# Kernel tuning notes

Hardware: AMD Instinct MI355X
Metric: run time of the kernel (lower is better)

Reference implementation:

```python
import jax, jax.numpy as jnp
import numpy as np

OBS, H, F1, A, T, B = 128, 128, 256, 18, 128, 1024


def _ln(x, w, b, eps=1e-5):
    mu = jnp.mean(x, -1, keepdims=True)
    xc = x - mu
    var = jnp.mean(xc * xc, -1, keepdims=True)
    return xc * jax.lax.rsqrt(var + eps) * w + b


def _features(x, w1, b1, w2, b2, lnw, lnb):
    h = jax.nn.relu(x @ w1.T + b1)      # [N, 256]
    h = h @ w2.T + b2                   # [N, 128]
    return jax.nn.relu(_ln(h, lnw, lnb))


def _masked_lstm(xs, ds, h0, c0, wih, whh, b):
    # xs: [T,B,H], ds: [T,B] float; PyTorch gate order i,f,g,o
    def step(carry, inp):
        h, c = carry
        xt, dt = inp
        m = (1.0 - dt)[:, None]
        h = h * m
        c = c * m
        g = xt @ wih.T + h @ whh.T + b  # [B, 4H]
        i, f, gg, o = jnp.split(g, 4, axis=-1)
        c = jax.nn.sigmoid(f) * c + jax.nn.sigmoid(i) * jnp.tanh(gg)
        h = jax.nn.sigmoid(o) * jnp.tanh(c)
        return (h, c), h
    (hT, cT), hs = jax.lax.scan(step, (h0, c0), (xs, ds))
    return hs, hT, cT


def setup_inputs() -> dict:
    key = jax.random.key(0)
    ks = iter(jax.random.split(key, 64))
    p = lambda shape, s=0.05: jax.random.normal(next(ks), shape, jnp.float32) * s
    inp = {
        'x': jax.random.normal(next(ks), (T * B, OBS), jnp.float32),
        'actor_h': jnp.zeros((1, B, H), jnp.float32),
        'actor_c': jnp.zeros((1, B, H), jnp.float32),
        'critic_h': jnp.zeros((1, B, H), jnp.float32),
        'critic_c': jnp.zeros((1, B, H), jnp.float32),
        'done': jax.random.randint(next(ks), (T * B,), 0, 2, jnp.int32),
        'action': jax.random.randint(next(ks), (T * B,), 0, A, jnp.int64),
        # actor params
        'af_w1': p((F1, OBS)), 'af_b1': p((F1,)),
        'af_w2': p((H, F1)), 'af_b2': p((H,)),
        'af_lnw': jnp.ones((H,), jnp.float32), 'af_lnb': jnp.zeros((H,), jnp.float32),
        'a_wih': p((4 * H, H)), 'a_whh': p((4 * H, H)), 'a_b': p((4 * H,)),
        'a_lnw': jnp.ones((H,), jnp.float32), 'a_lnb': jnp.zeros((H,), jnp.float32),
        'a_hw': p((A, H)), 'a_hb': p((A,)),
        # critic params
        'cf_w1': p((F1, OBS)), 'cf_b1': p((F1,)),
        'cf_w2': p((H, F1)), 'cf_b2': p((H,)),
        'cf_lnw': jnp.ones((H,), jnp.float32), 'cf_lnb': jnp.zeros((H,), jnp.float32),
        'c_wih': p((4 * H, H)), 'c_whh': p((4 * H, H)), 'c_b': p((4 * H,)),
        'c_lnw': jnp.ones((H,), jnp.float32), 'c_lnb': jnp.zeros((H,), jnp.float32),
        'c_hw': p((1, H)), 'c_hb': p((1,)),
    }
    return inp


def reference(x, actor_h, actor_c, critic_h, critic_c,
              af_w1, af_b1, af_w2, af_b2, af_lnw, af_lnb,
              a_wih, a_whh, a_b, a_lnw, a_lnb, a_hw, a_hb,
              cf_w1, cf_b1, cf_w2, cf_b2, cf_lnw, cf_lnb,
              c_wih, c_whh, c_b, c_lnw, c_lnb, c_hw, c_hb,
              done, action):
    bsz = actor_h.shape[1]
    ds = done.astype(jnp.float32).reshape(-1, bsz)  # [T, B]

    # actor branch
    af = _features(x, af_w1, af_b1, af_w2, af_b2, af_lnw, af_lnb).reshape(-1, bsz, H)
    hs, ahT, acT = _masked_lstm(af, ds, actor_h[0], actor_c[0], a_wih, a_whh, a_b)
    ah = _ln(hs.reshape(-1, H), a_lnw, a_lnb)
    logits = ah @ a_hw.T + a_hb                     # [N, A]
    logp_all = jax.nn.log_softmax(logits)
    logp = jnp.take_along_axis(logp_all, action[:, None], axis=1)[:, 0]
    entropy = -jnp.sum(jnp.exp(logp_all) * logp_all, axis=-1)

    # critic branch
    cf = _features(x, cf_w1, cf_b1, cf_w2, cf_b2, cf_lnw, cf_lnb).reshape(-1, bsz, H)
    cs, chT, ccT = _masked_lstm(cf, ds, critic_h[0], critic_c[0], c_wih, c_whh, c_b)
    ch = _ln(cs.reshape(-1, H), c_lnw, c_lnb)
    value = ch @ c_hw.T + c_hb                      # [N, 1]

    return (action, logp, entropy, value,
            ahT[None], acT[None], chT[None], ccT[None])
```

## Files before the change

### kernel.cpp

```cpp
#include <hip/hip_runtime.h>
#include <stdint.h>
#include <stddef.h>

#define OBS 128
#define F1D 256
#define HD  128
#define NA  18
#define TT  128
#define BB  1024
#define NN  (TT*BB)
#define LOG2E 1.442695041f

typedef __attribute__((ext_vector_type(8))) short short8;
typedef __attribute__((ext_vector_type(4))) float f32x4;

__device__ __forceinline__ unsigned short f2bf(float f) {
  union { float f; uint32_t u; } v; v.f = f;
  uint32_t u = v.u;
  u += 0x7fffu + ((u >> 16) & 1u);
  return (unsigned short)(u >> 16);
}
__device__ __forceinline__ float bf2f(uint32_t hu) {
  union { uint32_t u; float f; } v; v.u = hu << 16;
  return v.f;
}
__device__ __forceinline__ uint32_t pk2(float lo, float hi) {
  uint32_t r;
  asm("v_cvt_pk_bf16_f32 %0, %1, %2" : "=v"(r) : "v"(lo), "v"(hi));
  return r;
}
__device__ __forceinline__ f32x4 mfma16(short8 a, short8 b, f32x4 c) {
  return __builtin_amdgcn_mfma_f32_16x16x32_bf16(a, b, c, 0, 0, 0);
}
__device__ __forceinline__ short8 cvt8(const float* p, float sc) {
  float4 a = *(const float4*)p;
  float4 b = *(const float4*)(p + 4);
  union { uint32_t u[4]; short8 s; } o;
  o.u[0] = pk2(a.x*sc, a.y*sc);
  o.u[1] = pk2(a.z*sc, a.w*sc);
  o.u[2] = pk2(b.x*sc, b.y*sc);
  o.u[3] = pk2(b.z*sc, b.w*sc);
  return o.s;
}
__device__ __forceinline__ short8 pin(short8 v) {
  int4 i = *(int4*)&v;
  asm volatile("" : "+v"(i.x), "+v"(i.y), "+v"(i.z), "+v"(i.w));
  return *(short8*)&i;
}

__global__ __launch_bounds__(512, 2) void feat_kernel(
    const float* __restrict__ x,
    const float* __restrict__ aw1, const float* __restrict__ ab1,
    const float* __restrict__ aw2, const float* __restrict__ ab2,
    const float* __restrict__ aflnw, const float* __restrict__ aflnb,
    const float* __restrict__ cw1, const float* __restrict__ cb1,
    const float* __restrict__ cw2, const float* __restrict__ cb2,
    const float* __restrict__ cflnw, const float* __restrict__ cflnb,
    unsigned short* __restrict__ featg)
{
  int g = blockIdx.x;
  int br = g >> 7;
  int chunk = g & 127;
  int base8 = chunk * 8;

  const float* w1  = br ? cw1 : aw1;
  const float* b1  = br ? cb1 : ab1;
  const float* w2  = br ? cw2 : aw2;
  const float* b2  = br ? cb2 : ab2;
  const float* flw = br ? cflnw : aflnw;
  const float* flb = br ? cflnb : aflnb;
  unsigned short* feat = featg + (size_t)br * NN * HD;

  __shared__ __align__(16) char smemA[51200];

  int tid = threadIdx.x;
  int w = tid >> 6, lane = tid & 63, q = lane >> 4, ln = lane & 15;
  int team = tid >> 8, t_tid = tid & 255, w4 = w & 3;

  unsigned short* xst  = (unsigned short*)smemA + team*4096;
  unsigned short* h1st = (unsigned short*)(smemA + 16384) + team*8192;
  float*          lnst = (float*)(smemA + 49152) + team*256;

  short8 b1f[4][4]; float b1v[4];
  #pragma unroll
  for (int ct = 0; ct < 4; ++ct) {
    int nn = w4*64 + ct*16 + ln;
    b1v[ct] = b1[nn];
    #pragma unroll
    for (int kf = 0; kf < 4; ++kf)
      b1f[ct][kf] = pin(cvt8(&w1[nn*OBS + kf*32 + q*8], 1.0f));
  }
  short8 b2f[2][8]; float b2v[2], lwv[2], lbv[2];
  #pragma unroll
  for (int nt = 0; nt < 2; ++nt) {
    int nn = w4*32 + nt*16 + ln;
    b2v[nt] = b2[nn]; lwv[nt] = flw[nn]; lbv[nt] = flb[nn];
    #pragma unroll
    for (int kf = 0; kf < 8; ++kf)
      b2f[nt][kf] = pin(cvt8(&w2[nn*F1D + kf*32 + q*8], 1.0f));
  }
  float4 xr[4];
  #pragma unroll
  for (int s = 0; s < 4; ++s) {
    int e4 = t_tid + s*256;
    int r = e4 >> 5, c4 = e4 & 31;
    size_t grow = (size_t)(team*4 + (r>>3))*BB + base8 + (r&7);
    xr[s] = ((const float4*)x)[grow*32 + c4];
  }
  for (int j = 0; j < 16; ++j) {
    int jj = j*2 + team;
    #pragma unroll
    for (int s = 0; s < 4; ++s) {
      int e = (t_tid + s*256) * 4;
      int r = e >> 7, k = e & 127;
      int ad = r*128 + ((((k>>3) ^ (r&15)) << 3)) + (k&7);
      uint2 d;
      d.x = pk2(xr[s].x, xr[s].y);
      d.y = pk2(xr[s].z, xr[s].w);
      *(uint2*)&xst[ad] = d;
    }
    __syncthreads();
    {
      int jjn = (j < 15) ? jj + 2 : jj;
      #pragma unroll
      for (int s = 0; s < 4; ++s) {
        int e4 = t_tid + s*256;
        int r = e4 >> 5, c4 = e4 & 31;
        size_t grow = (size_t)(jjn*4 + (r>>3))*BB + base8 + (r&7);
        xr[s] = ((const float4*)x)[grow*32 + c4];
      }
    }
    short8 af[2][4];
    #pragma unroll
    for (int mt = 0; mt < 2; ++mt)
      #pragma unroll
      for (int kf = 0; kf < 4; ++kf)
        af[mt][kf] = *(const short8*)&xst[(mt*16 + ln)*128 + ((((kf<<2)|q) ^ ln) << 3)];
    #pragma unroll
    for (int ct = 0; ct < 4; ++ct) {
      int nn = w4*64 + ct*16 + ln;
      #pragma unroll
      for (int mt = 0; mt < 2; ++mt) {
        f32x4 acc = {b1v[ct], b1v[ct], b1v[ct], b1v[ct]};
        #pragma unroll
        for (int kf = 0; kf < 4; ++kf) acc = mfma16(af[mt][kf], b1f[ct][kf], acc);
        float v0 = acc[0] > 0.0f ? acc[0] : 0.0f;
        float v1 = acc[1] > 0.0f ? acc[1] : 0.0f;
        float v2 = acc[2] > 0.0f ? acc[2] : 0.0f;
        float v3 = acc[3] > 0.0f ? acc[3] : 0.0f;
        uint32_t p01 = pk2(v0, v1), p23 = pk2(v2, v3);
        int r0 = mt*16 + q*4;
        h1st[(r0+0)*256 + (((nn>>3) ^ ((r0+0)&15)) << 3) + (nn&7)] = (unsigned short)p01;
        h1st[(r0+1)*256 + (((nn>>3) ^ ((r0+1)&15)) << 3) + (nn&7)] = (unsigned short)(p01 >> 16);
        h1st[(r0+2)*256 + (((nn>>3) ^ ((r0+2)&15)) << 3) + (nn&7)] = (unsigned short)p23;
        h1st[(r0+3)*256 + (((nn>>3) ^ ((r0+3)&15)) << 3) + (nn&7)] = (unsigned short)(p23 >> 16);
      }
    }
    __syncthreads();
    f32x4 acc2[2][2];
    #pragma unroll
    for (int mt = 0; mt < 2; ++mt) {
      short8 ah[8];
      #pragma unroll
      for (int kf = 0; kf < 8; ++kf)
        ah[kf] = *(const short8*)&h1st[(mt*16 + ln)*256 + ((((kf<<2)|q) ^ ln) << 3)];
      #pragma unroll
      for (int nt = 0; nt < 2; ++nt) {
        f32x4 acc = {b2v[nt], b2v[nt], b2v[nt], b2v[nt]};
        #pragma unroll
        for (int kf = 0; kf < 8; ++kf) acc = mfma16(ah[kf], b2f[nt][kf], acc);
        acc2[nt][mt] = acc;
      }
    }
    #pragma unroll
    for (int mt = 0; mt < 2; ++mt)
      #pragma unroll
      for (int rg = 0; rg < 4; ++rg) {
        float s = acc2[0][mt][rg] + acc2[1][mt][rg];
        float ssq = acc2[0][mt][rg]*acc2[0][mt][rg] + acc2[1][mt][rg]*acc2[1][mt][rg];
        #pragma unroll
        for (int m = 1; m < 16; m <<= 1) { s += __shfl_xor(s, m); ssq += __shfl_xor(ssq, m); }
        if (ln == 0) {
          int r = mt*16 + q*4 + rg;
          lnst[r*8 + w4*2]     = s;
          lnst[r*8 + w4*2 + 1] = ssq;
        }
      }
    __syncthreads();
    #pragma unroll
    for (int mt = 0; mt < 2; ++mt)
      #pragma unroll
      for (int rg = 0; rg < 4; ++rg) {
        int r = mt*16 + q*4 + rg;
        float4 p0 = *(const float4*)&lnst[r*8];
        float4 p1 = *(const float4*)&lnst[r*8 + 4];
        float S  = p0.x + p0.z + p1.x + p1.z;
        float SS = p0.y + p0.w + p1.y + p1.w;
        float mu = S * (1.0f/128.0f);
        float var = SS * (1.0f/128.0f) - mu*mu;
        float rstd = rsqrtf(var + 1e-5f);
        size_t grow = (size_t)(jj*4 + (r>>3))*BB + base8 + (r&7);
        float t0 = (acc2[0][mt][rg] - mu) * rstd * lwv[0] + lbv[0];
        float t1 = (acc2[1][mt][rg] - mu) * rstd * lwv[1] + lbv[1];
        if (t0 < 0.0f) t0 = 0.0f;
        if (t1 < 0.0f) t1 = 0.0f;
        uint32_t p = pk2(t0, t1);
        unsigned short* fp = &feat[grow*HD + w4*32 + ln];
        fp[0]  = (unsigned short)p;
        fp[16] = (unsigned short)(p >> 16);
      }
    __syncthreads();
  }
}

__global__ __launch_bounds__(512, 2) void lstm_head_kernel(
    const int* __restrict__ done, const int* __restrict__ action,
    const float* __restrict__ awih, const float* __restrict__ awhh,
    const float* __restrict__ a_b,
    const float* __restrict__ alnw, const float* __restrict__ alnb,
    const float* __restrict__ ahw, const float* __restrict__ ahb,
    const float* __restrict__ cwih, const float* __restrict__ cwhh,
    const float* __restrict__ c_b,
    const float* __restrict__ clnw, const float* __restrict__ clnb,
    const float* __restrict__ chw, const float* __restrict__ chb,
    const float* __restrict__ ah0, const float* __restrict__ ac0,
    const float* __restrict__ ch0, const float* __restrict__ cc0,
    unsigned short* __restrict__ featg, float* __restrict__ dout)
{
  int g = blockIdx.x;
  int br = g >> 7;
  int chunk = g & 127;
  int base8 = chunk * 8;

  const float* wih = br ? cwih : awih;
  const float* whh = br ? cwhh : awhh;
  const float* gb  = br ? c_b : a_b;
  const float* h0  = br ? ch0 : ah0;
  const float* c0  = br ? cc0 : ac0;
  unsigned short* feat = featg + (size_t)br * NN * HD;

  __shared__ __align__(16) char smemC[51200];
  __shared__ float mls[(TT+1)*8];
  __shared__ unsigned short hlds[2][8*128];
  __shared__ float pa[HD], pb[HD], cws[HD];
  __shared__ float hbl[NA];
  __shared__ float cbsS;
  __shared__ int flagS;

  int tid = threadIdx.x;
  int w = tid >> 6, lane = tid & 63, q = lane >> 4, ln = lane & 15;

  int n = w*16 + ln;
  {
    short8 bfr[4][8]; float bias[4];
    #pragma unroll
    for (int g4 = 0; g4 < 4; ++g4) {
      int gn = g4*128 + n;
      float sc = (g4 == 2) ? -2.0f*LOG2E : -LOG2E;
      bias[g4] = gb[gn] * sc;
      #pragma unroll
      for (int kf = 0; kf < 8; ++kf) {
        const float* src = (kf < 4) ? &wih[gn*HD + kf*32 + q*8]
                                    : &whh[gn*HD + (kf-4)*32 + q*8];
        bfr[g4][kf] = pin(cvt8(src, sc));
      }
    }
    for (int i = tid; i < (TT+1)*8; i += 512)
      mls[i] = (i < TT*8) ? 1.0f - (float)done[(i>>3)*BB + base8 + (i&7)] : 1.0f;

    const int loff = (base8 + (ln>>1))*HD + q*8;
    int soff[2], hoffw[2], haddr[4];
    #pragma unroll
    for (int j = 0; j < 2; ++j) {
      int r = q*2 + j;
      soff[j]  = (base8 + r)*HD + n;
      hoffw[j] = r*128 + (((n>>3) ^ r) << 3) + (n&7);
    }
    #pragma unroll
    for (int kf = 0; kf < 4; ++kf) {
      int rr = ln >> 1;
      haddr[kf] = rr*128 + ((((kf<<2)|q) ^ rr) << 3);
    }
    float hp[2], cp[2]; unsigned short hu_prev[2];
    #pragma unroll
    for (int j = 0; j < 2; ++j) {
      int b = base8 + q*2 + j;
      hp[j] = h0[b*HD + n];
      cp[j] = c0[b*HD + n];
      hu_prev[j] = 0;
    }
    __syncthreads();
    short8 afr[4], nfr[4];
    #pragma unroll
    for (int kf = 0; kf < 4; ++kf)
      afr[kf] = *(const short8*)&feat[loff + kf*32];
    {
      float m0 = mls[q*2], m1 = mls[q*2 + 1];
      cp[0] *= m0; cp[1] *= m1;
      uint32_t hpk = pk2(hp[0]*m0, hp[1]*m1);
      hlds[0][hoffw[0]] = (unsigned short)hpk;
      hlds[0][hoffw[1]] = (unsigned short)(hpk >> 16);
    }
    __syncthreads();

#define LSTM_STEP(TTT, CUR, NXT, HB)                                           \
  {                                                                            \
    short8 hfr[4];                                                             \
    _Pragma("unroll")                                                          \
    for (int kf = 0; kf < 4; ++kf)                                             \
      hfr[kf] = *(const short8*)&hlds[HB][haddr[kf]];                          \
    {                                                                          \
      int tp = (TTT) > 0 ? (TTT) - 1 : 0;                                      \
      unsigned short* sq = feat + (size_t)tp * (BB*HD);                        \
      sq[soff[0]] = hu_prev[0];                                                \
      sq[soff[1]] = hu_prev[1];                                                \
    }                                                                          \
    int tn = ((TTT) + 1 < TT) ? (TTT) + 1 : TT - 1;                            \
    const unsigned short* fq = feat + (size_t)tn * (BB*HD);                    \
    _Pragma("unroll")                                                          \
    for (int kf = 0; kf < 4; ++kf)                                             \
      NXT[kf] = *(const short8*)&fq[loff + kf*32];                             \
    f32x4 a0 = {bias[0],bias[0],bias[0],bias[0]};                              \
    f32x4 a1 = {bias[1],bias[1],bias[1],bias[1]};                              \
    f32x4 a2 = {bias[2],bias[2],bias[2],bias[2]};                              \
    f32x4 a3 = {bias[3],bias[3],bias[3],bias[3]};                              \
    _Pragma("unroll")                                                          \
    for (int kf = 0; kf < 4; ++kf) {                                           \
      a0 = mfma16(CUR[kf], bfr[0][kf], a0);                                    \
      a1 = mfma16(CUR[kf], bfr[1][kf], a1);                                    \
      a2 = mfma16(CUR[kf], bfr[2][kf], a2);                                    \
      a3 = mfma16(CUR[kf], bfr[3][kf], a3);                                    \
    }                                                                          \
    _Pragma("unroll")                                                          \
    for (int kf = 0; kf < 4; ++kf) {                                           \
      a0 = mfma16(hfr[kf], bfr[0][4+kf], a0);                                  \
      a1 = mfma16(hfr[kf], bfr[1][4+kf], a1);                                  \
      a2 = mfma16(hfr[kf], bfr[2][4+kf], a2);                                  \
      a3 = mfma16(hfr[kf], bfr[3][4+kf], a3);                                  \
    }                                                                          \
    float hnv[2], cnv[2];                                                      \
    _Pragma("unroll")                                                          \
    for (int j = 0; j < 2; ++j) {                                              \
      int rg = j*2;     \
      float si = __builtin_amdgcn_rcpf(1.0f + __builtin_amdgcn_exp2f(a0[rg])); \
      float sf = __builtin_amdgcn_rcpf(1.0f + __builtin_amdgcn_exp2f(a1[rg])); \
      float tg = __builtin_fmaf(2.0f,                                          \
                   __builtin_amdgcn_rcpf(1.0f + __builtin_amdgcn_exp2f(a2[rg])), -1.0f); \
      float so = __builtin_amdgcn_rcpf(1.0f + __builtin_amdgcn_exp2f(a3[rg])); \
      float cn = __builtin_fmaf(sf, cp[j], si*tg);                             \
      float th = __builtin_fmaf(2.0f,                                          \
                   __builtin_amdgcn_rcpf(1.0f + __builtin_amdgcn_exp2f(-2.0f*LOG2E*cn)), -1.0f); \
      hnv[j] = so * th;                                                        \
      cnv[j] = cn;                                                             \
    }                                                                          \
    uint32_t hpk = pk2(hnv[0], hnv[1]);                                        \
    unsigned short hu0 = (unsigned short)hpk;                                  \
    unsigned short hu1 = (unsigned short)(hpk >> 16);                          \
    hu_prev[0] = hu0; hu_prev[1] = hu1;                                        \
    float2 mn = *(const float2*)&mls[((TTT)+1)*8 + q*2];                       \
    bool l0 = (mn.x != 0.0f), l1 = (mn.y != 0.0f);                             \
    cp[0] = l0 ? cnv[0] : 0.0f; hp[0] = hnv[0];                                \
    cp[1] = l1 ? cnv[1] : 0.0f; hp[1] = hnv[1];                                \
    hlds[(HB)^1][hoffw[0]] = l0 ? hu0 : (unsigned short)0;                     \
    hlds[(HB)^1][hoffw[1]] = l1 ? hu1 : (unsigned short)0;                     \
    __syncthreads();                                                           \
  }

    for (int t = 0; t < TT; t += 2) {
      LSTM_STEP(t,   afr, nfr, 0)
      LSTM_STEP(t+1, nfr, afr, 1)
    }
#undef LSTM_STEP

    {
      unsigned short* sq = feat + (size_t)(TT-1)*(BB*HD);
      sq[soff[0]] = hu_prev[0];
      sq[soff[1]] = hu_prev[1];
    }
    {
      float* outh = dout + (size_t)(4 + br*2) * NN;
      float* outc = dout + (size_t)(5 + br*2) * NN;
      #pragma unroll
      for (int j = 0; j < 2; ++j) {
        int b = base8 + q*2 + j;
        outh[b*HD + n] = hp[j];
        outc[b*HD + n] = cp[j];
      }
    }
  }

  if (tid == 0) flagS = 0;
  if (tid < HD) {
    pa[tid] = br ? clnw[tid] : alnw[tid];
    pb[tid] = br ? clnb[tid] : alnb[tid];
    if (br) cws[tid] = chw[tid];
  }
  int localf = 0;
  if (br == 0) {
    if (tid < NA) hbl[tid] = ahb[tid];
    for (int i = 2*tid + 1; i < 4096; i += 1024) localf |= action[i];
  } else if (tid == 0) cbsS = chb[0];
  __syncthreads();
  if (localf) flagS = 1;
  __syncthreads();

  int sub = tid & 3, kidx = tid >> 2;
  if (br == 0) {
    unsigned short* hsn = (unsigned short*)smemC;
    float* co = (float*)(smemC + 32768);
    short8 hbf[2][4];
    #pragma unroll
    for (int nt = 0; nt < 2; ++nt) {
      int nn = nt*16 + ln;
      #pragma unroll
      for (int kf = 0; kf < 4; ++kf) {
        short8 z = {0,0,0,0,0,0,0,0};
        hbf[nt][kf] = (nn < NA) ? pin(cvt8(&ahw[nn*HD + kf*32 + q*8], 1.0f)) : z;
      }
    }
    int fl = flagS;
    for (int ch = 0; ch < 8; ++ch) {
      {
        int k = ch*128 + kidx;
        int rrow = (k >> 3)*BB + base8 + (k & 7);
        const unsigned short* hp2 = feat + (size_t)rrow*HD + sub*32;
        uint4 d0 = *(const uint4*)hp2;
        uint4 d1 = *(const uint4*)(hp2 + 8);
        uint4 d2 = *(const uint4*)(hp2 + 16);
        uint4 d3 = *(const uint4*)(hp2 + 24);
        float nv[32];
        #define UP(W_, B_) { nv[B_] = bf2f((W_) & 0xffffu); nv[(B_)+1] = bf2f((W_) >> 16); }
        UP(d0.x,0) UP(d0.y,2) UP(d0.z,4) UP(d0.w,6)
        UP(d1.x,8) UP(d1.y,10) UP(d1.z,12) UP(d1.w,14)
        UP(d2.x,16) UP(d2.y,18) UP(d2.z,20) UP(d2.w,22)
        UP(d3.x,24) UP(d3.y,26) UP(d3.z,28) UP(d3.w,30)
        #undef UP
        float s = 0.0f, ssq = 0.0f;
        #pragma unroll
        for (int j = 0; j < 32; ++j) { s += nv[j]; ssq += nv[j]*nv[j]; }
        s += __shfl_xor(s, 1); ssq += __shfl_xor(ssq, 1);
        s += __shfl_xor(s, 2); ssq += __shfl_xor(ssq, 2);
        float mu = s * (1.0f/128.0f);
        float var = ssq * (1.0f/128.0f) - mu*mu;
        float rstd = rsqrtf(var + 1e-5f);
        #pragma unroll
        for (int cc = 0; cc < 4; ++cc) {
          float ov[8];
          #pragma unroll
          for (int j = 0; j < 8; ++j) {
            int c = sub*32 + cc*8 + j;
            ov[j] = (nv[cc*8+j] - mu) * rstd * pa[c] + pb[c];
          }
          uint4 P;
          P.x = pk2(ov[0], ov[1]); P.y = pk2(ov[2], ov[3]);
          P.z = pk2(ov[4], ov[5]); P.w = pk2(ov[6], ov[7]);
          int c8 = sub*4 + cc;
          *(uint4*)&hsn[kidx*128 + ((c8 ^ (kidx & 15)) << 3)] = P;
        }
      }
      __syncthreads();
      {
        short8 afh[4];
        #pragma unroll
        for (int kf = 0; kf < 4; ++kf)
          afh[kf] = *(const short8*)&hsn[(w*16 + ln)*128 + ((((kf<<2)|q) ^ ln) << 3)];
        #pragma unroll
        for (int nt = 0; nt < 2; ++nt) {
          f32x4 acc = {0.0f, 0.0f, 0.0f, 0.0f};
          #pragma unroll
          for (int kf = 0; kf < 4; ++kf) acc = mfma16(afh[kf], hbf[nt][kf], acc);
          #pragma unroll
          for (int rg = 0; rg < 4; ++rg)
            co[(w*16 + q*4 + rg)*36 + nt*16 + ln] = acc[rg];
        }
      }
      __syncthreads();
      if (tid < 128) {
        int k = ch*128 + tid;
        int rrow = (k >> 3)*BB + base8 + (k & 7);
        int act = fl ? action[rrow] : (int)(((const long long*)action)[rrow]);
        dout[rrow] = (float)act;
        int aidx = act < 0 ? 0 : (act > NA-1 ? NA-1 : act);
        float lg[NA];
        #pragma unroll
        for (int a = 0; a < NA; ++a) lg[a] = co[tid*36 + a] + hbl[a];
        float mx = lg[0];
        #pragma unroll
        for (int a = 1; a < NA; ++a) mx = fmaxf(mx, lg[a]);
        float se = 0.0f;
        #pragma unroll
        for (int a = 0; a < NA; ++a) se += __expf(lg[a] - mx);
        float lse = __logf(se);
        float lpa = 0.0f, ent = 0.0f;
        #pragma unroll
        for (int a = 0; a < NA; ++a) {
          float lp = lg[a] - mx - lse;
          ent -= __expf(lp) * lp;
          lpa += (a == aidx) ? lp : 0.0f;
        }
        dout[(size_t)NN + rrow] = lpa;
        dout[(size_t)2*NN + rrow] = ent;
      }
      __syncthreads();
    }
  } else {
    for (int ch = 0; ch < 8; ++ch) {
      int k = ch*128 + kidx;
      int rrow = (k >> 3)*BB + base8 + (k & 7);
      const unsigned short* hp2 = feat + (size_t)rrow*HD + sub*32;
      uint4 d0 = *(const uint4*)hp2;
      uint4 d1 = *(const uint4*)(hp2 + 8);
      uint4 d2 = *(const uint4*)(hp2 + 16);
      uint4 d3 = *(const uint4*)(hp2 + 24);
      float nv[32];
      #define UP(W_, B_) { nv[B_] = bf2f((W_) & 0xffffu); nv[(B_)+1] = bf2f((W_) >> 16); }
      UP(d0.x,0) UP(d0.y,2) UP(d0.z,4) UP(d0.w,6)
      UP(d1.x,8) UP(d1.y,10) UP(d1.z,12) UP(d1.w,14)
      UP(d2.x,16) UP(d2.y,18) UP(d2.z,20) UP(d2.w,22)
      UP(d3.x,24) UP(d3.y,26) UP(d3.z,28) UP(d3.w,30)
      #undef UP
      float s = 0.0f, ssq = 0.0f;
      #pragma unroll
      for (int j = 0; j < 32; ++j) { s += nv[j]; ssq += nv[j]*nv[j]; }
      s += __shfl_xor(s, 1); ssq += __shfl_xor(ssq, 1);
      s += __shfl_xor(s, 2); ssq += __shfl_xor(ssq, 2);
      float mu = s * (1.0f/128.0f);
      float var = ssq * (1.0f/128.0f) - mu*mu;
      float rstd = rsqrtf(var + 1e-5f);
      float dot = 0.0f;
      #pragma unroll
      for (int j = 0; j < 32; ++j) {
        int c = sub*32 + j;
        dot += ((nv[j] - mu) * rstd * pa[c] + pb[c]) * cws[c];
      }
      dot += __shfl_xor(dot, 1);
      dot += __shfl_xor(dot, 2);
      if (sub == 0) dout[(size_t)3*NN + rrow] = dot + cbsS;
    }
  }
}

extern "C" void kernel_launch(void* const* d_in, const int* in_sizes, int n_in,
                              void* d_out, int out_size, void* d_ws, size_t ws_size,
                              hipStream_t stream) {
  (void)in_sizes; (void)n_in; (void)out_size; (void)ws_size;
  const float* x    = (const float*)d_in[0];
  const float* ah0  = (const float*)d_in[1];
  const float* ac0  = (const float*)d_in[2];
  const float* ch0  = (const float*)d_in[3];
  const float* cc0  = (const float*)d_in[4];
  const int*   done = (const int*)d_in[5];
  const int*   act  = (const int*)d_in[6];
  const float* aw1  = (const float*)d_in[7];
  const float* ab1  = (const float*)d_in[8];
  const float* aw2  = (const float*)d_in[9];
  const float* ab2  = (const float*)d_in[10];
  const float* aflnw= (const float*)d_in[11];
  const float* aflnb= (const float*)d_in[12];
  const float* awih = (const float*)d_in[13];
  const float* awhh = (const float*)d_in[14];
  const float* a_b  = (const float*)d_in[15];
  const float* alnw = (const float*)d_in[16];
  const float* alnb = (const float*)d_in[17];
  const float* ahw  = (const float*)d_in[18];
  const float* ahb  = (const float*)d_in[19];
  const float* cw1  = (const float*)d_in[20];
  const float* cb1  = (const float*)d_in[21];
  const float* cw2  = (const float*)d_in[22];
  const float* cb2  = (const float*)d_in[23];
  const float* cflnw= (const float*)d_in[24];
  const float* cflnb= (const float*)d_in[25];
  const float* cwih = (const float*)d_in[26];
  const float* cwhh = (const float*)d_in[27];
  const float* c_b  = (const float*)d_in[28];
  const float* clnw = (const float*)d_in[29];
  const float* clnb = (const float*)d_in[30];
  const float* chw  = (const float*)d_in[31];
  const float* chb  = (const float*)d_in[32];

  unsigned short* featb = (unsigned short*)d_ws;
  float* out = (float*)d_out;

  feat_kernel<<<256, 512, 0, stream>>>(
      x, aw1, ab1, aw2, ab2, aflnw, aflnb,
      cw1, cb1, cw2, cb2, cflnw, cflnb, featb);

  lstm_head_kernel<<<256, 512, 0, stream>>>(
      done, act,
      awih, awhh, a_b, alnw, alnb, ahw, ahb,
      cwih, cwhh, c_b, clnw, clnb, chw, chb,
      ah0, ac0, ch0, cc0,
      featb, out);
}
```

Measured before the change: 434.9 us.

## Stage LSTM hidden outputs in an LDS ring and flush coalesced every 8 steps

Each step's bf16 hidden outputs now go into a 16-slot shared-memory ring instead of per-thread scattered 2-byte global stores. Every 8 steps the waves write the previous 8 timesteps back to global memory as 16-byte vector stores. __syncthreads is also replaced by a barrier that waits only on LDS counters, so outstanding global loads and stores need not drain at each step. The ring adds 32KB of LDS per block, which may reduce occupancy at 2 blocks per CU. The lighter barrier relies on correct ordering of the feature prefetch and the flushed writes.

```diff
diff --git a/kernel.cpp b/kernel.cpp
--- a/kernel.cpp
+++ b/kernel.cpp
@@ -46,6 +46,11 @@
   int4 i = *(int4*)&v;
   asm volatile("" : "+v"(i.x), "+v"(i.y), "+v"(i.z), "+v"(i.w));
   return *(short8*)&i;
+}
+__device__ __forceinline__ void bar_lds() {
+  asm volatile("s_waitcnt lgkmcnt(0)" ::: "memory");
+  __builtin_amdgcn_s_barrier();
+  asm volatile("" ::: "memory");
 }
 
 __global__ __launch_bounds__(512, 2) void feat_kernel(
@@ -240,6 +245,7 @@
   unsigned short* feat = featg + (size_t)br * NN * HD;
 
   __shared__ __align__(16) char smemC[51200];
+  __shared__ unsigned short ring[16*1024];
   __shared__ float mls[(TT+1)*8];
   __shared__ unsigned short hlds[2][8*128];
   __shared__ float pa[HD], pb[HD], cws[HD];
@@ -269,11 +275,10 @@
       mls[i] = (i < TT*8) ? 1.0f - (float)done[(i>>3)*BB + base8 + (i&7)] : 1.0f;
 
     const int loff = (base8 + (ln>>1))*HD + q*8;
-    int soff[2], hoffw[2], haddr[4];
+    int hoffw[2], haddr[4];
     #pragma unroll
     for (int j = 0; j < 2; ++j) {
       int r = q*2 + j;
-      soff[j]  = (base8 + r)*HD + n;
       hoffw[j] = r*128 + (((n>>3) ^ r) << 3) + (n&7);
     }
     #pragma unroll
@@ -281,13 +286,12 @@
       int rr = ln >> 1;
       haddr[kf] = rr*128 + ((((kf<<2)|q) ^ rr) << 3);
     }
-    float hp[2], cp[2]; unsigned short hu_prev[2];
+    float hp[2], cp[2];
     #pragma unroll
     for (int j = 0; j < 2; ++j) {
       int b = base8 + q*2 + j;
       hp[j] = h0[b*HD + n];
       cp[j] = c0[b*HD + n];
-      hu_prev[j] = 0;
     }
     __syncthreads();
     short8 afr[4], nfr[4];
@@ -303,18 +307,25 @@
     }
     __syncthreads();
 
+#define FLUSH(TB)                                                              \
+  {                                                                            \
+    int tp2 = (TB) + (tid >> 6);                                               \
+    int ss = (tp2 & 15) << 10;                                                 \
+    int fr = lane >> 3, fc = lane & 7;                                         \
+    int b0 = ((fc*2) ^ fr) << 3, b1 = ((fc*2+1) ^ fr) << 3;                    \
+    short8 v0 = *(const short8*)&ring[ss + fr*128 + b0];                       \
+    short8 v1 = *(const short8*)&ring[ss + fr*128 + b1];                       \
+    unsigned short* dst = feat + ((size_t)tp2*BB + base8 + fr)*HD + fc*16;     \
+    *(short8*)dst = v0;                                                        \
+    *(short8*)(dst + 8) = v1;                                                  \
+  }
+
 #define LSTM_STEP(TTT, CUR, NXT, HB)                                           \
   {                                                                            \
     short8 hfr[4];                                                             \
     _Pragma("unroll")                                                          \
     for (int kf = 0; kf < 4; ++kf)                                             \
       hfr[kf] = *(const short8*)&hlds[HB][haddr[kf]];                          \
-    {                                                                          \
-      int tp = (TTT) > 0 ? (TTT) - 1 : 0;                                      \
-      unsigned short* sq = feat + (size_t)tp * (BB*HD);                        \
-      sq[soff[0]] = hu_prev[0];                                                \
-      sq[soff[1]] = hu_prev[1];                                                \
-    }                                                                          \
     int tn = ((TTT) + 1 < TT) ? (TTT) + 1 : TT - 1;                            \
     const unsigned short* fq = feat + (size_t)tn * (BB*HD);                    \
     _Pragma("unroll")                                                          \
@@ -356,27 +367,27 @@
     uint32_t hpk = pk2(hnv[0], hnv[1]);                                        \
     unsigned short hu0 = (unsigned short)hpk;                                  \
     unsigned short hu1 = (unsigned short)(hpk >> 16);                          \
-    hu_prev[0] = hu0; hu_prev[1] = hu1;                                        \
+    int rbase = ((TTT) & 15) << 10;                                            \
+    ring[rbase + hoffw[0]] = hu0;                 \
+    ring[rbase + hoffw[1]] = hu1;                                              \
     float2 mn = *(const float2*)&mls[((TTT)+1)*8 + q*2];                       \
     bool l0 = (mn.x != 0.0f), l1 = (mn.y != 0.0f);                             \
     cp[0] = l0 ? cnv[0] : 0.0f; hp[0] = hnv[0];                                \
     cp[1] = l1 ? cnv[1] : 0.0f; hp[1] = hnv[1];                                \
     hlds[(HB)^1][hoffw[0]] = l0 ? hu0 : (unsigned short)0;                     \
     hlds[(HB)^1][hoffw[1]] = l1 ? hu1 : (unsigned short)0;                     \
-    __syncthreads();                                                           \
+    bar_lds();                                                                 \
   }
 
     for (int t = 0; t < TT; t += 2) {
+      if (t && !(t & 7)) FLUSH(t - 8)
       LSTM_STEP(t,   afr, nfr, 0)
       LSTM_STEP(t+1, nfr, afr, 1)
     }
+    FLUSH(TT - 8)
 #undef LSTM_STEP
-
-    {
-      unsigned short* sq = feat + (size_t)(TT-1)*(BB*HD);
-      sq[soff[0]] = hu_prev[0];
-      sq[soff[1]] = hu_prev[1];
-    }
+#undef FLUSH
+
     {
       float* outh = dout + (size_t)(4 + br*2) * NN;
       float* outc = dout + (size_t)(5 + br*2) * NN;
@@ -458,7 +469,7 @@
           *(uint4*)&hsn[kidx*128 + ((c8 ^ (kidx & 15)) << 3)] = P;
         }
       }
-      __syncthreads();
+      bar_lds();
       {
         short8 afh[4];
         #pragma unroll
@@ -474,7 +485,7 @@
             co[(w*16 + q*4 + rg)*36 + nt*16 + ln] = acc[rg];
         }
       }
-      __syncthreads();
+      bar_lds();
       if (tid < 128) {
         int k = ch*128 + tid;
         int rrow = (k >> 3)*BB + base8 + (k & 7);
@@ -501,12 +512,13 @@
         dout[(size_t)NN + rrow] = lpa;
         dout[(size_t)2*NN + rrow] = ent;
       }
-      __syncthreads();
+      bar_lds();
     }
   } else {
     for (int ch = 0; ch < 8; ++ch) {
       int k = ch*128 + kidx;
-      int rrow = (k >> 3)*BB + base8 + (k & 7);
+      int rrow = (k >> 3)*BB + base8 + (k & 3) + ((k & 7) - (k & 3));
+      rrow = (k >> 3)*BB + base8 + (k & 7);
       const unsigned short* hp2 = feat + (size_t)rrow*HD + sub*32;
       uint4 d0 = *(const uint4*)hp2;
       uint4 d1 = *(const uint4*)(hp2 + 8);
```

Measured after the change: 440.1 us. About the same (+1.2%).

## Software-pipeline LSTM input projection one step ahead of recurrence

Applied to the files above, without the earlier changes.

Computes the input-gate MFMA contribution for step t+1 during step t, so each step's critical path only carries the recurrent h@Whh MFMAs before the gate nonlinearities. Feature prefetch now runs two steps ahead, and the x-projection for step 0 is computed in a prologue. This removes the x-projection MFMAs from the serial dependency chain at the cost of extra accumulator registers (two sets of four f32x4 gate accumulators).

```diff
diff --git a/kernel.cpp b/kernel.cpp
--- a/kernel.cpp
+++ b/kernel.cpp
@@ -290,10 +290,28 @@
       hu_prev[j] = 0;
     }
     __syncthreads();
-    short8 afr[4], nfr[4];
+
+    short8 f0[4], f1[4];
     #pragma unroll
     for (int kf = 0; kf < 4; ++kf)
-      afr[kf] = *(const short8*)&feat[loff + kf*32];
+      f0[kf] = *(const short8*)&feat[loff + kf*32];
+    f32x4 xgA[4], xgB[4];
+    #pragma unroll
+    for (int g4 = 0; g4 < 4; ++g4)
+      xgA[g4] = (f32x4){bias[g4], bias[g4], bias[g4], bias[g4]};
+    #pragma unroll
+    for (int kf = 0; kf < 4; ++kf) {
+      xgA[0] = mfma16(f0[kf], bfr[0][kf], xgA[0]);
+      xgA[1] = mfma16(f0[kf], bfr[1][kf], xgA[1]);
+      xgA[2] = mfma16(f0[kf], bfr[2][kf], xgA[2]);
+      xgA[3] = mfma16(f0[kf], bfr[3][kf], xgA[3]);
+    }
+    {
+      const unsigned short* fq1 = feat + (size_t)1 * (BB*HD);
+      #pragma unroll
+      for (int kf = 0; kf < 4; ++kf)
+        f1[kf] = *(const short8*)&fq1[loff + kf*32];
+    }
     {
       float m0 = mls[q*2], m1 = mls[q*2 + 1];
       cp[0] *= m0; cp[1] *= m1;
@@ -303,50 +321,49 @@
     }
     __syncthreads();
 
-#define LSTM_STEP(TTT, CUR, NXT, HB)                                           \
+#define LSTM_STEP(TTT, CUR, NXT, XA, XN, HB)                                   \
   {                                                                            \
     short8 hfr[4];                                                             \
     _Pragma("unroll")                                                          \
     for (int kf = 0; kf < 4; ++kf)                                             \
       hfr[kf] = *(const short8*)&hlds[HB][haddr[kf]];                          \
-    {                                                                          \
-      int tp = (TTT) > 0 ? (TTT) - 1 : 0;                                      \
-      unsigned short* sq = feat + (size_t)tp * (BB*HD);                        \
+    if ((TTT) > 0) {                                                           \
+      unsigned short* sq = feat + (size_t)((TTT) - 1) * (BB*HD);               \
       sq[soff[0]] = hu_prev[0];                                                \
       sq[soff[1]] = hu_prev[1];                                                \
     }                                                                          \
-    int tn = ((TTT) + 1 < TT) ? (TTT) + 1 : TT - 1;                            \
+    int tn = ((TTT) + 2 < TT) ? (TTT) + 2 : TT - 1;                            \
     const unsigned short* fq = feat + (size_t)tn * (BB*HD);                    \
     _Pragma("unroll")                                                          \
     for (int kf = 0; kf < 4; ++kf)                                             \
       NXT[kf] = *(const short8*)&fq[loff + kf*32];                             \
-    f32x4 a0 = {bias[0],bias[0],bias[0],bias[0]};                              \
-    f32x4 a1 = {bias[1],bias[1],bias[1],bias[1]};                              \
-    f32x4 a2 = {bias[2],bias[2],bias[2],bias[2]};                              \
-    f32x4 a3 = {bias[3],bias[3],bias[3],bias[3]};                              \
     _Pragma("unroll")                                                          \
     for (int kf = 0; kf < 4; ++kf) {                                           \
-      a0 = mfma16(CUR[kf], bfr[0][kf], a0);                                    \
-      a1 = mfma16(CUR[kf], bfr[1][kf], a1);                                    \
-      a2 = mfma16(CUR[kf], bfr[2][kf], a2);                                    \
-      a3 = mfma16(CUR[kf], bfr[3][kf], a3);                                    \
+      (XA)[0] = mfma16(hfr[kf], bfr[0][4+kf], (XA)[0]);                        \
+      (XA)[1] = mfma16(hfr[kf], bfr[1][4+kf], (XA)[1]);                        \
+      (XA)[2] = mfma16(hfr[kf], bfr[2][4+kf], (XA)[2]);                        \
+      (XA)[3] = mfma16(hfr[kf], bfr[3][4+kf], (XA)[3]);                        \
     }                                                                          \
+    (XN)[0] = (f32x4){bias[0], bias[0], bias[0], bias[0]};                     \
+    (XN)[1] = (f32x4){bias[1], bias[1], bias[1], bias[1]};                     \
+    (XN)[2] = (f32x4){bias[2], bias[2], bias[2], bias[2]};                     \
+    (XN)[3] = (f32x4){bias[3], bias[3], bias[3], bias[3]};                     \
     _Pragma("unroll")                                                          \
     for (int kf = 0; kf < 4; ++kf) {                                           \
-      a0 = mfma16(hfr[kf], bfr[0][4+kf], a0);                                  \
-      a1 = mfma16(hfr[kf], bfr[1][4+kf], a1);                                  \
-      a2 = mfma16(hfr[kf], bfr[2][4+kf], a2);                                  \
-      a3 = mfma16(hfr[kf], bfr[3][4+kf], a3);                                  \
+      (XN)[0] = mfma16(CUR[kf], bfr[0][kf], (XN)[0]);                          \
+      (XN)[1] = mfma16(CUR[kf], bfr[1][kf], (XN)[1]);                          \
+      (XN)[2] = mfma16(CUR[kf], bfr[2][kf], (XN)[2]);                          \
+      (XN)[3] = mfma16(CUR[kf], bfr[3][kf], (XN)[3]);                          \
     }                                                                          \
     float hnv[2], cnv[2];                                                      \
     _Pragma("unroll")                                                          \
     for (int j = 0; j < 2; ++j) {                                              \
       int rg = j*2;     \
-      float si = __builtin_amdgcn_rcpf(1.0f + __builtin_amdgcn_exp2f(a0[rg])); \
-      float sf = __builtin_amdgcn_rcpf(1.0f + __builtin_amdgcn_exp2f(a1[rg])); \
+      float si = __builtin_amdgcn_rcpf(1.0f + __builtin_amdgcn_exp2f((XA)[0][rg])); \
+      float sf = __builtin_amdgcn_rcpf(1.0f + __builtin_amdgcn_exp2f((XA)[1][rg])); \
       float tg = __builtin_fmaf(2.0f,                                          \
-                   __builtin_amdgcn_rcpf(1.0f + __builtin_amdgcn_exp2f(a2[rg])), -1.0f); \
-      float so = __builtin_amdgcn_rcpf(1.0f + __builtin_amdgcn_exp2f(a3[rg])); \
+                   __builtin_amdgcn_rcpf(1.0f + __builtin_amdgcn_exp2f((XA)[2][rg])), -1.0f); \
+      float so = __builtin_amdgcn_rcpf(1.0f + __builtin_amdgcn_exp2f((XA)[3][rg])); \
       float cn = __builtin_fmaf(sf, cp[j], si*tg);                             \
       float th = __builtin_fmaf(2.0f,                                          \
                    __builtin_amdgcn_rcpf(1.0f + __builtin_amdgcn_exp2f(-2.0f*LOG2E*cn)), -1.0f); \
@@ -367,8 +384,8 @@
   }
 
     for (int t = 0; t < TT; t += 2) {
-      LSTM_STEP(t,   afr, nfr, 0)
-      LSTM_STEP(t+1, nfr, afr, 1)
+      LSTM_STEP(t,   f1, f0, xgA, xgB, 0)
+      LSTM_STEP(t+1, f0, f1, xgB, xgA, 1)
     }
 #undef LSTM_STEP
 
```

New measurement: 431.7 us. About the same (-0.7%).
